# Kernel tuning notes

Hardware: AMD Instinct MI355X
Metric: run time of the kernel (lower is better)

The kernel has to match this reference:

```python
import jax, jax.numpy as jnp
import numpy as np

C = 256
HEADS = 8
HD = C // HEADS
EPS = 1e-5


def _layernorm(x, g, b):
    mu = jnp.mean(x, axis=-1, keepdims=True)
    var = jnp.var(x, axis=-1, keepdims=True)
    return (x - mu) * jax.lax.rsqrt(var + EPS) * g + b


def setup_inputs() -> dict:
    key = jax.random.key(0)
    ks = jax.random.split(key, 16)
    s = 0.02
    return {
        "x": jax.random.normal(ks[0], (1, C, 64, 64), jnp.float32),
        "bn_gamma": 1.0 + s * jax.random.normal(ks[1], (C,), jnp.float32),
        "bn_beta": s * jax.random.normal(ks[2], (C,), jnp.float32),
        "bn_mean": s * jax.random.normal(ks[3], (C,), jnp.float32),
        "bn_var": jnp.ones((C,), jnp.float32),
        "w_in": s * jax.random.normal(ks[4], (C, C), jnp.float32),
        "b_in": jnp.zeros((C,), jnp.float32),
        "ln1_g": jnp.ones((C,), jnp.float32),
        "ln1_b": jnp.zeros((C,), jnp.float32),
        "w_qkv": s * jax.random.normal(ks[5], (3 * C, C), jnp.float32),
        "b_qkv": jnp.zeros((3 * C,), jnp.float32),
        "w_ap": s * jax.random.normal(ks[6], (C, C), jnp.float32),
        "b_ap": jnp.zeros((C,), jnp.float32),
        "ln2_g": jnp.ones((C,), jnp.float32),
        "ln2_b": jnp.zeros((C,), jnp.float32),
        "w_ff1": s * jax.random.normal(ks[7], (4 * C, C), jnp.float32),
        "b_ff1": jnp.zeros((4 * C,), jnp.float32),
        "w_ff2": s * jax.random.normal(ks[8], (C, 4 * C), jnp.float32),
        "b_ff2": jnp.zeros((C,), jnp.float32),
        "w_out": s * jax.random.normal(ks[9], (C, C), jnp.float32),
        "b_out": jnp.zeros((C,), jnp.float32),
    }


def reference(x, bn_gamma, bn_beta, bn_mean, bn_var, w_in, b_in,
              ln1_g, ln1_b, w_qkv, b_qkv, w_ap, b_ap,
              ln2_g, ln2_b, w_ff1, b_ff1, w_ff2, b_ff2, w_out, b_out):
    b, c, h, w = x.shape
    t = h * w
    x_in = x
    # BatchNorm2d (eval mode: running stats)
    xn = (x - bn_mean[None, :, None, None]) * jax.lax.rsqrt(bn_var + EPS)[None, :, None, None]
    xn = xn * bn_gamma[None, :, None, None] + bn_beta[None, :, None, None]
    # proj_in 1x1 conv -> tokens [b, t, c]
    tok = xn.reshape(b, c, t).transpose(0, 2, 1)
    tok = tok @ w_in.T + b_in
    # transformer block (depth=1)
    y = _layernorm(tok, ln1_g, ln1_b)  # norm1
    qkv = y @ w_qkv.T + b_qkv  # [b, t, 3c], channel split (3, H, hd)
    qkv = qkv.reshape(b, t, 3, HEADS, HD)
    q = qkv[:, :, 0].transpose(0, 2, 1, 3)  # [b, H, t, hd]
    k = qkv[:, :, 1].transpose(0, 2, 1, 3)
    v = qkv[:, :, 2].transpose(0, 2, 1, 3)
    scale = HD ** (-0.5)
    attn = jax.nn.softmax(jnp.einsum('bhqd,bhkd->bhqk', q, k) * scale, axis=-1)
    o = jnp.einsum('bhqk,bhkd->bhqd', attn, v)  # [b, H, t, hd]
    o = o.transpose(0, 2, 1, 3).reshape(b, t, c)  # channels ordered (H, hd)
    o = o @ w_ap.T + b_ap  # attn proj 1x1
    attn_out = o + y  # VanillaAttention residual adds its (normed) input
    tok = tok + attn_out
    # FFN
    z = _layernorm(tok, ln2_g, ln2_b)
    z = jax.nn.gelu(z @ w_ff1.T + b_ff1, approximate=False)
    tok = tok + (z @ w_ff2.T + b_ff2)
    # back to image, proj_out 1x1, outer residual
    x4 = tok.transpose(0, 2, 1).reshape(b, c, h, w)
    out = jnp.einsum('oc,bchw->bohw', w_out, x4) + b_out[None, :, None, None]
    return out + x_in
```

## Files before the change

### kernel.cpp

```cpp
#include <hip/hip_runtime.h>
#include <math.h>

#define T_TOK 4096
#define C_DIM 256
#define EPSF  1e-5f
#define SC_QL (0.17677669529663687f * 1.4426950408889634f)

typedef short  bf16x8  __attribute__((ext_vector_type(8)));
typedef float  f32x4   __attribute__((ext_vector_type(4)));
typedef ushort ushort8 __attribute__((ext_vector_type(8)));
typedef unsigned uint4v __attribute__((ext_vector_type(4)));
typedef unsigned uint2v __attribute__((ext_vector_type(2)));

__device__ __forceinline__ short f2bf(float f) {
    unsigned u = __builtin_bit_cast(unsigned, f);
    unsigned r = (u + 0x7FFFu + ((u >> 16) & 1u)) >> 16;
    return (short)r;
}
__device__ __forceinline__ float bf2f(ushort u) {
    return __builtin_bit_cast(float, ((unsigned)u) << 16);
}
__device__ __forceinline__ unsigned pk_bf16(float a, float b) {
    const unsigned ua = __builtin_bit_cast(unsigned, a) + 0x8000u;
    const unsigned ub = __builtin_bit_cast(unsigned, b) + 0x8000u;
    return __builtin_amdgcn_perm(ub, ua, 0x07060302u);
}
__device__ __forceinline__ unsigned cvtpk_bf16(float a, float b) {
    unsigned r;
    asm("v_cvt_pk_bf16_f32 %0, %1, %2" : "=v"(r) : "v"(a), "v"(b));
    return r;
}
__device__ __forceinline__ void plswap32(unsigned &a, unsigned &b) {
    asm("v_permlane32_swap_b32 %0, %1" : "+v"(a), "+v"(b));
}
__device__ __forceinline__ void plswap16(unsigned &a, unsigned &b) {
    asm("v_permlane16_swap_b32 %0, %1" : "+v"(a), "+v"(b));
}
template <int CTRL>
__device__ __forceinline__ float dppf(float x) {
    return __builtin_bit_cast(float,
        __builtin_amdgcn_mov_dpp(__builtin_bit_cast(int, x), CTRL, 0xF, 0xF, true));
}
__device__ __forceinline__ float rowsum16(float x) {
    x += dppf<0xB1>(x);
    x += dppf<0x4E>(x);
    x += dppf<0x141>(x);
    x += dppf<0x140>(x);
    return x;
}
#define MFMA16(a, b, c) __builtin_amdgcn_mfma_f32_16x16x32_bf16(a, b, c, 0, 0, 0)

__global__ __launch_bounds__(256) void prep_kernel(
    const float* __restrict__ w_in, const float* __restrict__ w_qkv,
    const float* __restrict__ w_ap, const float* __restrict__ w_ff1,
    const float* __restrict__ w_ff2, const float* __restrict__ w_out,
    const float* __restrict__ b_qkv, ushort* __restrict__ wbuf,
    float* __restrict__ bqs,
    const float* __restrict__ x, const float* __restrict__ gamma,
    const float* __restrict__ beta, const float* __restrict__ mean,
    const float* __restrict__ var, ushort* __restrict__ tin)
{
    __shared__ float tile[32][33];
    if (blockIdx.x < 896) {
        const int gid = blockIdx.x * 256 + threadIdx.x;
        const int e0 = gid * 4;
        const float* src; int off; float sc = 1.f;
        if (e0 < 65536)       { src = w_in;  off = e0; }
        else if (e0 < 262144) { src = w_qkv; off = e0 - 65536; if (off < 65536) sc = SC_QL; }
        else if (e0 < 327680) { src = w_ap;  off = e0 - 262144; }
        else if (e0 < 589824) { src = w_ff1; off = e0 - 327680; }
        else if (e0 < 851968) { src = w_ff2; off = e0 - 589824; }
        else                  { src = w_out; off = e0 - 851968; }
        const float4 v = *(const float4*)(src + off);
        ushort4 o;
        o.x = (ushort)f2bf(v.x * sc); o.y = (ushort)f2bf(v.y * sc);
        o.z = (ushort)f2bf(v.z * sc); o.w = (ushort)f2bf(v.w * sc);
        *(ushort4*)(wbuf + e0) = o;
        if (gid < 192) {
            const float s2 = (gid < 64) ? SC_QL : 1.f;
            float4 b = ((const float4*)b_qkv)[gid];
            b.x *= s2; b.y *= s2; b.z *= s2; b.w *= s2;
            ((float4*)bqs)[gid] = b;
        }
    } else {
        const int bidx = blockIdx.x - 896;
        const int t0 = (bidx & 127) * 32, c0 = (bidx >> 7) * 32;
        const int tx = threadIdx.x & 31, ty = threadIdx.x >> 5;
#pragma unroll
        for (int i = 0; i < 32; i += 8) {
            const int c = c0 + ty + i;
            const float a = rsqrtf(var[c] + EPSF) * gamma[c];
            const float d = beta[c] - mean[c] * a;
            tile[ty + i][tx] = x[c * T_TOK + t0 + tx] * a + d;
        }
        __syncthreads();
#pragma unroll
        for (int i = 0; i < 32; i += 8) {
            const int t = t0 + ty + i;
            tin[t * C_DIM + c0 + tx] = (ushort)f2bf(tile[tx][ty + i]);
        }
    }
}

__global__ __launch_bounds__(1024) void fused_pre(
    const ushort* __restrict__ tin, const ushort* __restrict__ wb_in,
    const float* __restrict__ b_in, const float* __restrict__ ln1_g,
    const float* __restrict__ ln1_b, const ushort* __restrict__ wb_qkv,
    const float* __restrict__ bqs, float* __restrict__ tok0,
    float* __restrict__ yout, ushort* __restrict__ qkvb)
{
    __shared__ ushort Atile[16 * 264];
    __shared__ ushort Ytile[16 * 264];
    __shared__ float  red[16][16][2];
    const int t0 = blockIdx.x * 16;
    const int tid = threadIdx.x, wv = tid >> 6, lane = tid & 63;
    const int c = lane & 15, g = lane >> 4;

    {
        const int r = tid >> 6, c0 = (tid & 63) * 4;
        *(ushort4*)&Atile[r * 264 + c0] = *(const ushort4*)(tin + (size_t)(t0 + r) * 256 + c0);
    }
    __syncthreads();

    f32x4 accp = {};
#pragma unroll
    for (int kc = 0; kc < 8; ++kc) {
        const bf16x8 af = *(const bf16x8*)&Atile[c * 264 + kc * 32 + g * 8];
        const bf16x8 bfv = *(const bf16x8*)(wb_in +
            (size_t)(wv * 16 + c) * 256 + kc * 32 + g * 8);
        accp = MFMA16(af, bfv, accp);
    }
    const int colp = wv * 16 + c;
    {
        const float bb = b_in[colp];
        float vs[4], s1[4], s2[4];
#pragma unroll
        for (int rr = 0; rr < 4; ++rr) {
            const float v = accp[rr] + bb;
            vs[rr] = v; s1[rr] = v; s2[rr] = v * v;
            tok0[(size_t)(t0 + 4 * g + rr) * 256 + colp] = v;
        }
#pragma unroll
        for (int rr = 0; rr < 4; ++rr) { s1[rr] = rowsum16(s1[rr]); s2[rr] = rowsum16(s2[rr]); }
        if (c == 0) {
#pragma unroll
            for (int rr = 0; rr < 4; ++rr) {
                red[wv][4 * g + rr][0] = s1[rr];
                red[wv][4 * g + rr][1] = s2[rr];
            }
        }
        __syncthreads();
        if (tid < 32) {
            const int row = tid >> 1, j = tid & 1;
            float s = 0.f;
#pragma unroll
            for (int w = 0; w < 16; ++w) s += red[w][row][j];
            red[0][row][j] = s;
        }
        __syncthreads();
        const float gg = ln1_g[colp], lb = ln1_b[colp];
#pragma unroll
        for (int rr = 0; rr < 4; ++rr) {
            const int row = 4 * g + rr;
            const float mu = red[0][row][0] * (1.0f / 256.0f);
            const float var = red[0][row][1] * (1.0f / 256.0f) - mu * mu;
            const float rs = rsqrtf(var + EPSF);
            const float yv = (vs[rr] - mu) * rs * gg + lb;
            yout[(size_t)(t0 + row) * 256 + colp] = yv;
            Ytile[row * 264 + colp] = (ushort)f2bf(yv);
        }
    }
    __syncthreads();

    f32x4 accq[3] = {};
#pragma unroll
    for (int kc = 0; kc < 8; ++kc) {
        const bf16x8 af = *(const bf16x8*)&Ytile[c * 264 + kc * 32 + g * 8];
#pragma unroll
        for (int nf = 0; nf < 3; ++nf) {
            const bf16x8 bfv = *(const bf16x8*)(wb_qkv +
                (size_t)(wv * 48 + nf * 16 + c) * 256 + kc * 32 + g * 8);
            accq[nf] = MFMA16(af, bfv, accq[nf]);
        }
    }
#pragma unroll
    for (int nf = 0; nf < 3; ++nf) {
        const int col = wv * 48 + nf * 16 + c;
        const float bb = bqs[col];
#pragma unroll
        for (int rr = 0; rr < 4; ++rr)
            qkvb[(size_t)(t0 + 4 * g + rr) * 768 + col] = (ushort)f2bf(accq[nf][rr] + bb);
    }
}

#define KS   40
#define VTS  72

__global__ __launch_bounds__(256) void attn_mfma(
    const ushort* __restrict__ qkv, ushort* __restrict__ o1,
    ushort* __restrict__ o2, ushort* __restrict__ o3,
    ushort* __restrict__ o4, float* __restrict__ lpart, int h0)
{
    const int h    = h0 + blockIdx.y;
    const int q0   = blockIdx.x << 6;
    const int qrt  = blockIdx.z;
    const int tid  = threadIdx.x;
    const int wv   = tid >> 6, lane = tid & 63;
    const int c    = lane & 15, g = lane >> 4;

    __shared__ ushort Ks[2][64 * KS];
    __shared__ ushort Vt[2][32 * VTS];

    const bf16x8 qf = *(const bf16x8*)(qkv + (size_t)(q0 + wv * 16 + c) * 768 + h * 32 + g * 8);

    bf16x8 ones;
#pragma unroll
    for (int i = 0; i < 8; ++i) ones[i] = (short)0x3F80;

    f32x4 oacc0 = {0.f, 0.f, 0.f, 0.f};
    f32x4 oacc1 = {0.f, 0.f, 0.f, 0.f};
    f32x4 oaccl = {0.f, 0.f, 0.f, 0.f};

    const int kr = wv * 16 + c, kc = g * 8;
    const int vp = tid & 31, vd = (tid >> 5) * 4;
    const ushort* kbase = qkv + 256 + h * 32;
    const ushort* vbase = qkv + 512 + h * 32;

    const int kt0 = qrt * 16, kt1 = kt0 + 16;

    {
        const ushort8 kv = *(const ushort8*)(kbase + ((size_t)kt0 * 64 + kr) * 768 + kc);
        const uint2v va = *(const uint2v*)(vbase + ((size_t)kt0 * 64 + 2 * vp) * 768 + vd);
        const uint2v vb = *(const uint2v*)(vbase + ((size_t)kt0 * 64 + 2 * vp + 1) * 768 + vd);
        *(ushort8*)&Ks[0][kr * KS + kc] = kv;
        unsigned* vtp = (unsigned*)&Vt[0][0];
        vtp[(vd + 0) * (VTS / 2) + vp] = __builtin_amdgcn_perm(vb.x, va.x, 0x05040100u);
        vtp[(vd + 1) * (VTS / 2) + vp] = __builtin_amdgcn_perm(vb.x, va.x, 0x07060302u);
        vtp[(vd + 2) * (VTS / 2) + vp] = __builtin_amdgcn_perm(vb.y, va.y, 0x05040100u);
        vtp[(vd + 3) * (VTS / 2) + vp] = __builtin_amdgcn_perm(vb.y, va.y, 0x07060302u);
    }
    ushort8 kpre = *(const ushort8*)(kbase + ((size_t)(kt0 + 1) * 64 + kr) * 768 + kc);
    uint2v vpre0 = *(const uint2v*)(vbase + ((size_t)(kt0 + 1) * 64 + 2 * vp) * 768 + vd);
    uint2v vpre1 = *(const uint2v*)(vbase + ((size_t)(kt0 + 1) * 64 + 2 * vp + 1) * 768 + vd);
    __syncthreads();

    int p = 0;
    for (int kt = kt0; kt < kt1; ++kt) {
        const ushort* ks = &Ks[p][0];
        const ushort* vt = &Vt[p][0];
        const bf16x8 k0 = *(const bf16x8*)&ks[(0 * 16 + c) * KS + g * 8];
        const bf16x8 k1 = *(const bf16x8*)&ks[(1 * 16 + c) * KS + g * 8];
        const bf16x8 k2 = *(const bf16x8*)&ks[(2 * 16 + c) * KS + g * 8];
        const bf16x8 k3 = *(const bf16x8*)&ks[(3 * 16 + c) * KS + g * 8];

        if (kt + 1 < kt1) {
            *(ushort8*)&Ks[p ^ 1][kr * KS + kc] = kpre;
            unsigned* vtp = (unsigned*)&Vt[p ^ 1][0];
            vtp[(vd + 0) * (VTS / 2) + vp] = __builtin_amdgcn_perm(vpre1.x, vpre0.x, 0x05040100u);
            vtp[(vd + 1) * (VTS / 2) + vp] = __builtin_amdgcn_perm(vpre1.x, vpre0.x, 0x07060302u);
            vtp[(vd + 2) * (VTS / 2) + vp] = __builtin_amdgcn_perm(vpre1.y, vpre0.y, 0x05040100u);
            vtp[(vd + 3) * (VTS / 2) + vp] = __builtin_amdgcn_perm(vpre1.y, vpre0.y, 0x07060302u);
            if (kt + 2 < kt1) {
                const size_t t2 = (size_t)(kt + 2) * 64;
                kpre  = *(const ushort8*)(kbase + (t2 + kr) * 768 + kc);
                vpre0 = *(const uint2v*)(vbase + (t2 + 2 * vp) * 768 + vd);
                vpre1 = *(const uint2v*)(vbase + (t2 + 2 * vp + 1) * 768 + vd);
            }
        }

        const f32x4 zz = {0.f, 0.f, 0.f, 0.f};
        const f32x4 s0 = MFMA16(k0, qf, zz);
        const f32x4 s1 = MFMA16(k1, qf, zz);
        const f32x4 s2 = MFMA16(k2, qf, zz);
        const f32x4 s3 = MFMA16(k3, qf, zz);

        unsigned w00 = cvtpk_bf16(__builtin_amdgcn_exp2f(s0[0]), __builtin_amdgcn_exp2f(s0[1]));
        unsigned w01 = cvtpk_bf16(__builtin_amdgcn_exp2f(s0[2]), __builtin_amdgcn_exp2f(s0[3]));
        unsigned w10 = cvtpk_bf16(__builtin_amdgcn_exp2f(s1[0]), __builtin_amdgcn_exp2f(s1[1]));
        unsigned w11 = cvtpk_bf16(__builtin_amdgcn_exp2f(s1[2]), __builtin_amdgcn_exp2f(s1[3]));
        unsigned w20 = cvtpk_bf16(__builtin_amdgcn_exp2f(s2[0]), __builtin_amdgcn_exp2f(s2[1]));
        unsigned w21 = cvtpk_bf16(__builtin_amdgcn_exp2f(s2[2]), __builtin_amdgcn_exp2f(s2[3]));
        unsigned w30 = cvtpk_bf16(__builtin_amdgcn_exp2f(s3[0]), __builtin_amdgcn_exp2f(s3[1]));
        unsigned w31 = cvtpk_bf16(__builtin_amdgcn_exp2f(s3[2]), __builtin_amdgcn_exp2f(s3[3]));

        plswap32(w00, w10); plswap16(w00, w10);
        plswap32(w01, w11); plswap16(w01, w11);
        plswap32(w20, w30); plswap16(w20, w30);
        plswap32(w21, w31); plswap16(w21, w31);
        const uint4v u0 = {w00, w01, w10, w11};
        const uint4v u1 = {w20, w21, w30, w31};
        const bf16x8 pa0 = __builtin_bit_cast(bf16x8, u0);
        const bf16x8 pa1 = __builtin_bit_cast(bf16x8, u1);

        {
            const bf16x8 va0 = *(const bf16x8*)&vt[(c)      * VTS + 0 * 32 + g * 8];
            const bf16x8 vb0 = *(const bf16x8*)&vt[(16 + c) * VTS + 0 * 32 + g * 8];
            oacc0 = MFMA16(pa0, va0, oacc0);
            oacc1 = MFMA16(pa0, vb0, oacc1);
            oaccl = MFMA16(pa0, ones, oaccl);
            const bf16x8 va1 = *(const bf16x8*)&vt[(c)      * VTS + 1 * 32 + g * 8];
            const bf16x8 vb1 = *(const bf16x8*)&vt[(16 + c) * VTS + 1 * 32 + g * 8];
            oacc0 = MFMA16(pa1, va1, oacc0);
            oacc1 = MFMA16(pa1, vb1, oacc1);
            oaccl = MFMA16(pa1, ones, oaccl);
        }
        p ^= 1;
        __syncthreads();
    }

    {
        ushort* ob = (qrt & 2) ? ((qrt & 1) ? o4 : o3) : ((qrt & 1) ? o2 : o1);
        ushort* op = ob + (size_t)(q0 + wv * 16) * 256 + h * 32;
#pragma unroll
        for (int rr = 0; rr < 4; ++rr) {
            op[(4 * g + rr) * 256 + c]      = (ushort)f2bf(oacc0[rr]);
            op[(4 * g + rr) * 256 + 16 + c] = (ushort)f2bf(oacc1[rr]);
        }
        if (c == 0) {
#pragma unroll
            for (int rr = 0; rr < 4; ++rr)
                lpart[(size_t)(q0 + wv * 16 + 4 * g + rr) * 32 + qrt * 8 + h] = oaccl[rr];
        }
    }
}

__global__ __launch_bounds__(1024) void fused_mid(
    const ushort* __restrict__ o1, const ushort* __restrict__ o2,
    const ushort* __restrict__ o3, const ushort* __restrict__ o4,
    const float* __restrict__ lpart, const ushort* __restrict__ wb_ap,
    const float* __restrict__ b_ap, const float* __restrict__ yin,
    const float* __restrict__ tok0, const float* __restrict__ ln2_g,
    const float* __restrict__ ln2_b, const ushort* __restrict__ wb_ff1,
    const float* __restrict__ b_ff1, float* __restrict__ tok1,
    ushort* __restrict__ zbuf)
{
    __shared__ ushort Otile[16 * 264];
    __shared__ ushort Ztile[16 * 264];
    __shared__ float  red[16][16][2];
    const int t0 = blockIdx.x * 16;
    const int tid = threadIdx.x, wv = tid >> 6, lane = tid & 63;
    const int c = lane & 15, g = lane >> 4;

    {
        const int r = tid >> 6, c0 = (tid & 63) * 4;
        const int h = (tid & 63) >> 3;
        const float* lp = lpart + (size_t)(t0 + r) * 32;
        const float inv = 1.0f / (lp[h] + lp[8 + h] + lp[16 + h] + lp[24 + h]);
        const size_t idx = (size_t)(t0 + r) * 256 + c0;
        const ushort4 a = *(const ushort4*)(o1 + idx);
        const ushort4 b = *(const ushort4*)(o2 + idx);
        const ushort4 d = *(const ushort4*)(o3 + idx);
        const ushort4 e = *(const ushort4*)(o4 + idx);
        unsigned w[2];
        w[0] = pk_bf16((bf2f(a.x) + bf2f(b.x) + bf2f(d.x) + bf2f(e.x)) * inv,
                       (bf2f(a.y) + bf2f(b.y) + bf2f(d.y) + bf2f(e.y)) * inv);
        w[1] = pk_bf16((bf2f(a.z) + bf2f(b.z) + bf2f(d.z) + bf2f(e.z)) * inv,
                       (bf2f(a.w) + bf2f(b.w) + bf2f(d.w) + bf2f(e.w)) * inv);
        *(ushort4*)&Otile[r * 264 + c0] = *(ushort4*)w;
    }
    __syncthreads();

    f32x4 accp = {};
#pragma unroll
    for (int kc = 0; kc < 8; ++kc) {
        const bf16x8 af = *(const bf16x8*)&Otile[c * 264 + kc * 32 + g * 8];
        const bf16x8 bfv = *(const bf16x8*)(wb_ap +
            (size_t)(wv * 16 + c) * 256 + kc * 32 + g * 8);
        accp = MFMA16(af, bfv, accp);
    }
    const int colp = wv * 16 + c;
    {
        const float bb = b_ap[colp];
        float vs[4], s1[4], s2[4];
#pragma unroll
        for (int rr = 0; rr < 4; ++rr) {
            const size_t idx = (size_t)(t0 + 4 * g + rr) * 256 + colp;
            const float v = accp[rr] + bb + yin[idx] + tok0[idx];
            vs[rr] = v; s1[rr] = v; s2[rr] = v * v;
            tok1[idx] = v;
        }
#pragma unroll
        for (int rr = 0; rr < 4; ++rr) { s1[rr] = rowsum16(s1[rr]); s2[rr] = rowsum16(s2[rr]); }
        if (c == 0) {
#pragma unroll
            for (int rr = 0; rr < 4; ++rr) {
                red[wv][4 * g + rr][0] = s1[rr];
                red[wv][4 * g + rr][1] = s2[rr];
            }
        }
        __syncthreads();
        if (tid < 32) {
            const int row = tid >> 1, j = tid & 1;
            float s = 0.f;
#pragma unroll
            for (int w = 0; w < 16; ++w) s += red[w][row][j];
            red[0][row][j] = s;
        }
        __syncthreads();
        const float gg = ln2_g[colp], lb = ln2_b[colp];
#pragma unroll
        for (int rr = 0; rr < 4; ++rr) {
            const int row = 4 * g + rr;
            const float mu = red[0][row][0] * (1.0f / 256.0f);
            const float var = red[0][row][1] * (1.0f / 256.0f) - mu * mu;
            const float rs = rsqrtf(var + EPSF);
            const float zv = (vs[rr] - mu) * rs * gg + lb;
            Ztile[row * 264 + colp] = (ushort)f2bf(zv);
        }
    }
    __syncthreads();

    f32x4 accf[4] = {};
#pragma unroll
    for (int kc = 0; kc < 8; ++kc) {
        const bf16x8 af = *(const bf16x8*)&Ztile[c * 264 + kc * 32 + g * 8];
#pragma unroll
        for (int nf = 0; nf < 4; ++nf) {
            const bf16x8 bfv = *(const bf16x8*)(wb_ff1 +
                (size_t)(wv * 64 + nf * 16 + c) * 256 + kc * 32 + g * 8);
            accf[nf] = MFMA16(af, bfv, accf[nf]);
        }
    }
#pragma unroll
    for (int nf = 0; nf < 4; ++nf) {
        const int col = wv * 64 + nf * 16 + c;
        const float bb = b_ff1[col];
#pragma unroll
        for (int rr = 0; rr < 4; ++rr) {
            float v = accf[nf][rr] + bb;
            v = 0.5f * v * (1.0f + erff(v * 0.70710678118654752f));
            zbuf[(size_t)(t0 + 4 * g + rr) * 1024 + col] = (ushort)f2bf(v);
        }
    }
}

__global__ __launch_bounds__(1024) void fused_post(
    const ushort* __restrict__ zbuf, const ushort* __restrict__ wb_ff2,
    const float* __restrict__ b_ff2, const float* __restrict__ tok1,
    const ushort* __restrict__ wb_out, const float* __restrict__ b_out,
    const float* __restrict__ x, float* __restrict__ out)
{
    __shared__ ushort Ztile[16 * 1032];
    __shared__ ushort T2tile[16 * 264];
    const int t0 = blockIdx.x * 16;
    const int tid = threadIdx.x, wv = tid >> 6, lane = tid & 63;
    const int c = lane & 15, g = lane >> 4;

    {
        const int r = tid >> 6, c0 = (tid & 63) * 16;
        *(ushort8*)&Ztile[r * 1032 + c0] =
            *(const ushort8*)(zbuf + (size_t)(t0 + r) * 1024 + c0);
        *(ushort8*)&Ztile[r * 1032 + c0 + 8] =
            *(const ushort8*)(zbuf + (size_t)(t0 + r) * 1024 + c0 + 8);
    }
    __syncthreads();

    f32x4 accf = {};
#pragma unroll
    for (int kc = 0; kc < 32; ++kc) {
        const bf16x8 af = *(const bf16x8*)&Ztile[c * 1032 + kc * 32 + g * 8];
        const bf16x8 bfv = *(const bf16x8*)(wb_ff2 +
            (size_t)(wv * 16 + c) * 1024 + kc * 32 + g * 8);
        accf = MFMA16(af, bfv, accf);
    }
    {
        const int col = wv * 16 + c;
        const float bb = b_ff2[col];
#pragma unroll
        for (int rr = 0; rr < 4; ++rr) {
            const size_t idx = (size_t)(t0 + 4 * g + rr) * 256 + col;
            const float v = accf[rr] + bb + tok1[idx];
            T2tile[(4 * g + rr) * 264 + col] = (ushort)f2bf(v);
        }
    }
    __syncthreads();

    f32x4 acco = {};
#pragma unroll
    for (int kc = 0; kc < 8; ++kc) {
        const bf16x8 bfr = *(const bf16x8*)&T2tile[c * 264 + kc * 32 + g * 8];
        const bf16x8 afr = *(const bf16x8*)(wb_out +
            (size_t)(wv * 16 + c) * 256 + kc * 32 + g * 8);
        acco = MFMA16(afr, bfr, acco);
    }
#pragma unroll
    for (int rr = 0; rr < 4; ++rr) {
        const int och = wv * 16 + 4 * g + rr;
        const size_t idx = (size_t)och * T_TOK + t0 + c;
        out[idx] = acco[rr] + b_out[och] + x[idx];
    }
}

extern "C" void kernel_launch(void* const* d_in, const int* in_sizes, int n_in,
                              void* d_out, int out_size, void* d_ws, size_t ws_size,
                              hipStream_t stream)
{
    const float* x     = (const float*)d_in[0];
    const float* bn_g  = (const float*)d_in[1];
    const float* bn_b  = (const float*)d_in[2];
    const float* bn_m  = (const float*)d_in[3];
    const float* bn_v  = (const float*)d_in[4];
    const float* w_in  = (const float*)d_in[5];
    const float* b_in  = (const float*)d_in[6];
    const float* ln1_g = (const float*)d_in[7];
    const float* ln1_b = (const float*)d_in[8];
    const float* w_qkv = (const float*)d_in[9];
    const float* b_qkv = (const float*)d_in[10];
    const float* w_ap  = (const float*)d_in[11];
    const float* b_ap  = (const float*)d_in[12];
    const float* ln2_g = (const float*)d_in[13];
    const float* ln2_b = (const float*)d_in[14];
    const float* w_ff1 = (const float*)d_in[15];
    const float* b_ff1 = (const float*)d_in[16];
    const float* w_ff2 = (const float*)d_in[17];
    const float* b_ff2 = (const float*)d_in[18];
    const float* w_out = (const float*)d_in[19];
    const float* b_out = (const float*)d_in[20];
    float* out = (float*)d_out;
    float* ws  = (float*)d_ws;

    const size_t MF = 1u << 20;
    float*  tok0   = ws;
    float*  y      = ws + MF;
    float*  tok1   = ws + 2 * MF;
    ushort* qkv_bf = (ushort*)(ws + 3 * MF);
    ushort* zbuf   = (ushort*)(ws + 4 * MF + MF / 2);
    ushort* tin_bf = (ushort*)(ws + 6 * MF + MF / 2);
    ushort* o1p    = tin_bf;
    ushort* o2p    = (ushort*)(ws + 7 * MF);
    ushort* o3p    = (ushort*)(ws + 7 * MF + MF / 2);
    ushort* o4p    = (ushort*)(ws + 8 * MF);
    float*  lpart  = ws + 8 * MF + MF / 2;
    ushort* wbuf   = (ushort*)(ws + 8 * MF + MF / 2 + 131072);
    const ushort* wb_in  = wbuf;
    const ushort* wb_qkv = wbuf + 65536;
    const ushort* wb_ap  = wbuf + 262144;
    const ushort* wb_ff1 = wbuf + 327680;
    const ushort* wb_ff2 = wbuf + 589824;
    const ushort* wb_out = wbuf + 851968;
    float* bqs = (float*)(wbuf + 917504);

    prep_kernel<<<1920, 256, 0, stream>>>(w_in, w_qkv, w_ap, w_ff1, w_ff2, w_out,
                                          b_qkv, wbuf, bqs,
                                          x, bn_g, bn_b, bn_m, bn_v, tin_bf);
    fused_pre<<<256, 1024, 0, stream>>>(tin_bf, wb_in, b_in, ln1_g, ln1_b,
                                        wb_qkv, bqs, tok0, y, qkv_bf);
    attn_mfma<<<dim3(64, 4, 4), 256, 0, stream>>>(qkv_bf, o1p, o2p, o3p, o4p, lpart, 0);
    attn_mfma<<<dim3(64, 4, 4), 256, 0, stream>>>(qkv_bf, o1p, o2p, o3p, o4p, lpart, 4);
    fused_mid<<<256, 1024, 0, stream>>>(o1p, o2p, o3p, o4p, lpart, wb_ap, b_ap,
                                        y, tok0, ln2_g, ln2_b, wb_ff1, b_ff1,
                                        tok1, zbuf);
    fused_post<<<256, 1024, 0, stream>>>(zbuf, wb_ff2, b_ff2, tok1, wb_out, b_out,
                                         x, out);
}
```

Baseline: 214.2 us.

## Fuse FFN2 and output projection into mid kernel; launch attention once

Merges the fused_mid and fused_post kernels into a single fused_tail kernel. The GELU activations and post-attention tokens now stay in shared memory and registers instead of going through global buffers (zbuf, tok1). The two attention launches that each covered four heads are also combined into one launch covering all eight heads. This removes global round-trips and launch gaps. In exchange it raises shared-memory use per block, which may reduce occupancy for the larger kernel.

```diff
diff --git a/kernel.cpp b/kernel.cpp
--- a/kernel.cpp
+++ b/kernel.cpp
@@ -199,9 +199,9 @@
 __global__ __launch_bounds__(256) void attn_mfma(
     const ushort* __restrict__ qkv, ushort* __restrict__ o1,
     ushort* __restrict__ o2, ushort* __restrict__ o3,
-    ushort* __restrict__ o4, float* __restrict__ lpart, int h0)
+    ushort* __restrict__ o4, float* __restrict__ lpart)
 {
-    const int h    = h0 + blockIdx.y;
+    const int h    = blockIdx.y;
     const int q0   = blockIdx.x << 6;
     const int qrt  = blockIdx.z;
     const int tid  = threadIdx.x;
@@ -324,18 +324,22 @@
     }
 }
 
-__global__ __launch_bounds__(1024) void fused_mid(
+__global__ __launch_bounds__(1024) void fused_tail(
     const ushort* __restrict__ o1, const ushort* __restrict__ o2,
     const ushort* __restrict__ o3, const ushort* __restrict__ o4,
     const float* __restrict__ lpart, const ushort* __restrict__ wb_ap,
     const float* __restrict__ b_ap, const float* __restrict__ yin,
     const float* __restrict__ tok0, const float* __restrict__ ln2_g,
     const float* __restrict__ ln2_b, const ushort* __restrict__ wb_ff1,
-    const float* __restrict__ b_ff1, float* __restrict__ tok1,
-    ushort* __restrict__ zbuf)
+    const float* __restrict__ b_ff1, const ushort* __restrict__ wb_ff2,
+    const float* __restrict__ b_ff2, const ushort* __restrict__ wb_out,
+    const float* __restrict__ b_out, const float* __restrict__ x,
+    float* __restrict__ out)
 {
     __shared__ ushort Otile[16 * 264];
     __shared__ ushort Ztile[16 * 264];
+    __shared__ ushort Zbig[16 * 1032];
+    __shared__ ushort T2tile[16 * 264];
     __shared__ float  red[16][16][2];
     const int t0 = blockIdx.x * 16;
     const int tid = threadIdx.x, wv = tid >> 6, lane = tid & 63;
@@ -369,15 +373,15 @@
         accp = MFMA16(af, bfv, accp);
     }
     const int colp = wv * 16 + c;
+    float vsave[4];
     {
         const float bb = b_ap[colp];
-        float vs[4], s1[4], s2[4];
+        float s1[4], s2[4];
 #pragma unroll
         for (int rr = 0; rr < 4; ++rr) {
             const size_t idx = (size_t)(t0 + 4 * g + rr) * 256 + colp;
             const float v = accp[rr] + bb + yin[idx] + tok0[idx];
-            vs[rr] = v; s1[rr] = v; s2[rr] = v * v;
-            tok1[idx] = v;
+            vsave[rr] = v; s1[rr] = v; s2[rr] = v * v;
         }
 #pragma unroll
         for (int rr = 0; rr < 4; ++rr) { s1[rr] = rowsum16(s1[rr]); s2[rr] = rowsum16(s2[rr]); }
@@ -404,73 +408,52 @@
             const float mu = red[0][row][0] * (1.0f / 256.0f);
             const float var = red[0][row][1] * (1.0f / 256.0f) - mu * mu;
             const float rs = rsqrtf(var + EPSF);
-            const float zv = (vs[rr] - mu) * rs * gg + lb;
+            const float zv = (vsave[rr] - mu) * rs * gg + lb;
             Ztile[row * 264 + colp] = (ushort)f2bf(zv);
         }
     }
     __syncthreads();
 
-    f32x4 accf[4] = {};
-#pragma unroll
-    for (int kc = 0; kc < 8; ++kc) {
-        const bf16x8 af = *(const bf16x8*)&Ztile[c * 264 + kc * 32 + g * 8];
+    {
+        f32x4 accf[4] = {};
+#pragma unroll
+        for (int kc = 0; kc < 8; ++kc) {
+            const bf16x8 af = *(const bf16x8*)&Ztile[c * 264 + kc * 32 + g * 8];
+#pragma unroll
+            for (int nf = 0; nf < 4; ++nf) {
+                const bf16x8 bfv = *(const bf16x8*)(wb_ff1 +
+                    (size_t)(wv * 64 + nf * 16 + c) * 256 + kc * 32 + g * 8);
+                accf[nf] = MFMA16(af, bfv, accf[nf]);
+            }
+        }
 #pragma unroll
         for (int nf = 0; nf < 4; ++nf) {
-            const bf16x8 bfv = *(const bf16x8*)(wb_ff1 +
-                (size_t)(wv * 64 + nf * 16 + c) * 256 + kc * 32 + g * 8);
-            accf[nf] = MFMA16(af, bfv, accf[nf]);
-        }
-    }
-#pragma unroll
-    for (int nf = 0; nf < 4; ++nf) {
-        const int col = wv * 64 + nf * 16 + c;
-        const float bb = b_ff1[col];
+            const int col = wv * 64 + nf * 16 + c;
+            const float bb = b_ff1[col];
+#pragma unroll
+            for (int rr = 0; rr < 4; ++rr) {
+                float v = accf[nf][rr] + bb;
+                v = 0.5f * v * (1.0f + erff(v * 0.70710678118654752f));
+                Zbig[(4 * g + rr) * 1032 + col] = (ushort)f2bf(v);
+            }
+        }
+    }
+    __syncthreads();
+
+    {
+        f32x4 accf = {};
+#pragma unroll
+        for (int kc = 0; kc < 32; ++kc) {
+            const bf16x8 af = *(const bf16x8*)&Zbig[c * 1032 + kc * 32 + g * 8];
+            const bf16x8 bfv = *(const bf16x8*)(wb_ff2 +
+                (size_t)(wv * 16 + c) * 1024 + kc * 32 + g * 8);
+            accf = MFMA16(af, bfv, accf);
+        }
+        const float bb = b_ff2[colp];
 #pragma unroll
         for (int rr = 0; rr < 4; ++rr) {
-            float v = accf[nf][rr] + bb;
-            v = 0.5f * v * (1.0f + erff(v * 0.70710678118654752f));
-            zbuf[(size_t)(t0 + 4 * g + rr) * 1024 + col] = (ushort)f2bf(v);
-        }
-    }
-}
-
-__global__ __launch_bounds__(1024) void fused_post(
-    const ushort* __restrict__ zbuf, const ushort* __restrict__ wb_ff2,
-    const float* __restrict__ b_ff2, const float* __restrict__ tok1,
-    const ushort* __restrict__ wb_out, const float* __restrict__ b_out,
-    const float* __restrict__ x, float* __restrict__ out)
-{
-    __shared__ ushort Ztile[16 * 1032];
-    __shared__ ushort T2tile[16 * 264];
-    const int t0 = blockIdx.x * 16;
-    const int tid = threadIdx.x, wv = tid >> 6, lane = tid & 63;
-    const int c = lane & 15, g = lane >> 4;
-
-    {
-        const int r = tid >> 6, c0 = (tid & 63) * 16;
-        *(ushort8*)&Ztile[r * 1032 + c0] =
-            *(const ushort8*)(zbuf + (size_t)(t0 + r) * 1024 + c0);
-        *(ushort8*)&Ztile[r * 1032 + c0 + 8] =
-            *(const ushort8*)(zbuf + (size_t)(t0 + r) * 1024 + c0 + 8);
-    }
-    __syncthreads();
-
-    f32x4 accf = {};
-#pragma unroll
-    for (int kc = 0; kc < 32; ++kc) {
-        const bf16x8 af = *(const bf16x8*)&Ztile[c * 1032 + kc * 32 + g * 8];
-        const bf16x8 bfv = *(const bf16x8*)(wb_ff2 +
-            (size_t)(wv * 16 + c) * 1024 + kc * 32 + g * 8);
-        accf = MFMA16(af, bfv, accf);
-    }
-    {
-        const int col = wv * 16 + c;
-        const float bb = b_ff2[col];
-#pragma unroll
-        for (int rr = 0; rr < 4; ++rr) {
-            const size_t idx = (size_t)(t0 + 4 * g + rr) * 256 + col;
-            const float v = accf[rr] + bb + tok1[idx];
-            T2tile[(4 * g + rr) * 264 + col] = (ushort)f2bf(v);
+            const float v = accf[rr] + bb + vsave[rr];
+            T2tile[(4 * g + rr) * 264 + colp] = (ushort)f2bf(v);
         }
     }
     __syncthreads();
@@ -522,9 +505,7 @@
     const size_t MF = 1u << 20;
     float*  tok0   = ws;
     float*  y      = ws + MF;
-    float*  tok1   = ws + 2 * MF;
     ushort* qkv_bf = (ushort*)(ws + 3 * MF);
-    ushort* zbuf   = (ushort*)(ws + 4 * MF + MF / 2);
     ushort* tin_bf = (ushort*)(ws + 6 * MF + MF / 2);
     ushort* o1p    = tin_bf;
     ushort* o2p    = (ushort*)(ws + 7 * MF);
@@ -545,11 +526,8 @@
                                           x, bn_g, bn_b, bn_m, bn_v, tin_bf);
     fused_pre<<<256, 1024, 0, stream>>>(tin_bf, wb_in, b_in, ln1_g, ln1_b,
                                         wb_qkv, bqs, tok0, y, qkv_bf);
-    attn_mfma<<<dim3(64, 4, 4), 256, 0, stream>>>(qkv_bf, o1p, o2p, o3p, o4p, lpart, 0);
-    attn_mfma<<<dim3(64, 4, 4), 256, 0, stream>>>(qkv_bf, o1p, o2p, o3p, o4p, lpart, 4);
-    fused_mid<<<256, 1024, 0, stream>>>(o1p, o2p, o3p, o4p, lpart, wb_ap, b_ap,
-                                        y, tok0, ln2_g, ln2_b, wb_ff1, b_ff1,
-                                        tok1, zbuf);
-    fused_post<<<256, 1024, 0, stream>>>(zbuf, wb_ff2, b_ff2, tok1, wb_out, b_out,
-                                         x, out);
-}
+    attn_mfma<<<dim3(64, 8, 4), 256, 0, stream>>>(qkv_bf, o1p, o2p, o3p, o4p, lpart);
+    fused_tail<<<256, 1024, 0, stream>>>(o1p, o2p, o3p, o4p, lpart, wb_ap, b_ap,
+                                         y, tok0, ln2_g, ln2_b, wb_ff1, b_ff1,
+                                         wb_ff2, b_ff2, wb_out, b_out, x, out);
+}
```

Result: faster. 208.1 us (-2.8%).
